# Kernel tuning notes

Hardware: AMD Instinct MI355X
Metric: run time of the kernel (lower is better)

Reference implementation:

```python
import jax, jax.numpy as jnp
import numpy as np

N_FEATURES = 1024
N_HEADS = 16
DEPTH = N_FEATURES // N_HEADS


def setup_inputs() -> dict:
    key = jax.random.key(0)
    ks = jax.random.split(key, 12)
    B, S, D = 2, 2048, N_FEATURES
    s = 1.0 / np.sqrt(D)
    return {
        "q": jax.random.normal(ks[0], (B, S, D), jnp.float32),
        "k": jax.random.normal(ks[1], (B, S, D), jnp.float32),
        "v": jax.random.normal(ks[2], (B, S, D), jnp.float32),
        "w_q": jax.random.normal(ks[3], (D, D), jnp.float32) * s,
        "b_q": jnp.zeros((D,), jnp.float32),
        "w_k": jax.random.normal(ks[4], (D, D), jnp.float32) * s,
        "b_k": jnp.zeros((D,), jnp.float32),
        "w_v": jax.random.normal(ks[5], (D, D), jnp.float32) * s,
        "b_v": jnp.zeros((D,), jnp.float32),
        "w_o": jax.random.normal(ks[6], (D, D), jnp.float32) * s,
        "b_o": jnp.zeros((D,), jnp.float32),
    }


def _split_heads(x):
    # [B, S, D] -> [B, H, S, depth]
    B, S, _ = x.shape
    return x.reshape(B, S, N_HEADS, DEPTH).transpose(0, 2, 1, 3)


def reference(q, k, v, w_q, b_q, w_k, b_k, w_v, b_v, w_o, b_o):
    B, S, D = q.shape
    qh = _split_heads(q @ w_q + b_q)  # [B,H,S,d]
    kh = _split_heads(k @ w_k + b_k)
    vh = _split_heads(v @ w_v + b_v)
    scale = 1.0 / jnp.sqrt(jnp.asarray(DEPTH, jnp.float32))
    logits = jnp.einsum("bhqd,bhkd->bhqk", qh, kh) * scale  # [B,H,S,S]
    attn_weights = jax.nn.softmax(logits, axis=-1)
    attn = jnp.einsum("bhqk,bhkd->bhqd", attn_weights, vh)
    concat = attn.transpose(0, 2, 1, 3).reshape(B, S, D)
    output = concat @ w_o + b_o
    return output, attn_weights
```

## Files before the change

### kernel.cpp

```cpp
#include <hip/hip_runtime.h>

typedef __attribute__((ext_vector_type(8))) short short8;
typedef __attribute__((ext_vector_type(4))) float f32x4;

#define MFMA_BF16(A,B,C) __builtin_amdgcn_mfma_f32_16x16x32_bf16((A),(B),(C),0,0,0)

__device__ __forceinline__ unsigned short f2bu(float f) {
  unsigned int u = __float_as_uint(f);
  u += 0x7fffu + ((u >> 16) & 1u);
  return (unsigned short)(u >> 16);
}
__device__ __forceinline__ float bu2f(unsigned short u) {
  return __uint_as_float(((unsigned int)u) << 16);
}
__device__ __forceinline__ void gload16(const void* g, void* l) {
  __builtin_amdgcn_global_load_lds(
      (const __attribute__((address_space(1))) void*)g,
      (__attribute__((address_space(3))) void*)l, 16, 0, 0);
}

__global__ __launch_bounds__(256) void cvt_bf16_kernel(const float* __restrict__ in,
                                                       unsigned short* __restrict__ out,
                                                       int n4) {
  int i = blockIdx.x * 256 + threadIdx.x;
  if (i >= n4) return;
  const float4 v = reinterpret_cast<const float4*>(in)[i];
  ushort4 o;
  o.x = f2bu(v.x); o.y = f2bu(v.y); o.z = f2bu(v.z); o.w = f2bu(v.w);
  reinterpret_cast<ushort4*>(out)[i] = o;
}

__global__ __launch_bounds__(256) void transpose_cvt_kernel(const float* __restrict__ w,
                                                            unsigned short* __restrict__ wt) {
  __shared__ float t[32][33];
  const int bx = blockIdx.x * 32;
  const int by = blockIdx.y * 32;
  const int tx = threadIdx.x & 31, ty = threadIdx.x >> 5;
  for (int j = 0; j < 4; ++j)
    t[ty + 8 * j][tx] = w[(size_t)(bx + ty + 8 * j) * 1024 + by + tx];
  __syncthreads();
  for (int j = 0; j < 4; ++j)
    wt[(size_t)(by + ty + 8 * j) * 1024 + bx + tx] = f2bu(t[tx][ty + 8 * j]);
}

template <int OUT_MODE>
__global__ __launch_bounds__(512) void gemm_bt(
    const unsigned short* __restrict__ A, const unsigned short* __restrict__ Wt,
    const float* __restrict__ bias, void* __restrict__ Cout) {
  __shared__ unsigned short g_lds[2][16384];
  const int M0 = blockIdx.x * 128, N0 = blockIdx.y * 128;
  const int tid = threadIdx.x, lane = tid & 63, wid = tid >> 6;
  const int lr = lane & 15, lg = lane >> 4;
  const int wr = wid >> 2, wc = wid & 3;
  const int srow = lane >> 3, slot = lane & 7;
  f32x4 acc[4][2];
#pragma unroll
  for (int m = 0; m < 4; ++m)
#pragma unroll
    for (int n = 0; n < 2; ++n) acc[m][n] = (f32x4){0.f, 0.f, 0.f, 0.f};

#define G_STAGE(buf, kk)                                                             \
  {                                                                                  \
    _Pragma("unroll") for (int i_ = 0; i_ < 2; ++i_) {                               \
      int idx_ = wid * 2 + i_;                                                       \
      int row_ = idx_ * 8 + srow;                                                    \
      int gs_ = slot ^ (row_ & 7);                                                   \
      gload16(&A[(size_t)(M0 + row_) * 1024 + (kk) + gs_ * 8],                       \
              (char*)&g_lds[buf][0] + idx_ * 1024);                                  \
      gload16(&Wt[(size_t)(N0 + row_) * 1024 + (kk) + gs_ * 8],                      \
              (char*)&g_lds[buf][0] + 16384 + idx_ * 1024);                          \
    }                                                                                \
  }

  G_STAGE(0, 0);
  __syncthreads();
  for (int kt = 0; kt < 16; ++kt) {
    const int cur = kt & 1;
    if (kt < 15) G_STAGE(cur ^ 1, (kt + 1) * 64);
    short8 af[4][2], bf[2][2];
#pragma unroll
    for (int m = 0; m < 4; ++m)
#pragma unroll
      for (int kh = 0; kh < 2; ++kh) {
        int row = wr * 64 + m * 16 + lr;
        int s = (kh * 4 + lg) ^ (row & 7);
        af[m][kh] = *reinterpret_cast<const short8*>((const char*)&g_lds[cur][0] + row * 128 + s * 16);
      }
#pragma unroll
    for (int n = 0; n < 2; ++n)
#pragma unroll
      for (int kh = 0; kh < 2; ++kh) {
        int row = wc * 32 + n * 16 + lr;
        int s = (kh * 4 + lg) ^ (row & 7);
        bf[n][kh] = *reinterpret_cast<const short8*>((const char*)&g_lds[cur][0] + 16384 + row * 128 + s * 16);
      }
#pragma unroll
    for (int kh = 0; kh < 2; ++kh)
#pragma unroll
      for (int m = 0; m < 4; ++m)
#pragma unroll
        for (int n = 0; n < 2; ++n)
          acc[m][n] = MFMA_BF16(af[m][kh], bf[n][kh], acc[m][n]);
    __syncthreads();
  }

  if (OUT_MODE != 2) {
#pragma unroll
    for (int m = 0; m < 4; ++m)
#pragma unroll
      for (int n = 0; n < 2; ++n)
#pragma unroll
        for (int r = 0; r < 4; ++r) {
          int grow = M0 + wr * 64 + m * 16 + lg * 4 + r;
          int gcol = N0 + wc * 32 + n * 16 + lr;
          float vv = acc[m][n][r] + bias[gcol];
          if (OUT_MODE == 1)
            reinterpret_cast<float*>(Cout)[(size_t)grow * 1024 + gcol] = vv;
          else
            reinterpret_cast<unsigned short*>(Cout)[(size_t)grow * 1024 + gcol] = f2bu(vv);
        }
  } else {
    unsigned short* t = &g_lds[0][0];
#pragma unroll
    for (int m = 0; m < 4; ++m)
#pragma unroll
      for (int n = 0; n < 2; ++n) {
        int ch = wc * 32 + n * 16 + lr;
        int s4 = wr * 64 + m * 16 + lg * 4;
        int sb = (s4 * 2) ^ ((ch & 7) << 4);
        ushort4 pk;
        pk.x = f2bu(acc[m][n][0] + bias[N0 + ch]);
        pk.y = f2bu(acc[m][n][1] + bias[N0 + ch]);
        pk.z = f2bu(acc[m][n][2] + bias[N0 + ch]);
        pk.w = f2bu(acc[m][n][3] + bias[N0 + ch]);
        *reinterpret_cast<ushort4*>((char*)t + ch * 256 + sb) = pk;
      }
    __syncthreads();
    unsigned short* Vt = (unsigned short*)Cout;
    const int ch = tid >> 2, sc = tid & 3;
    const int bb = M0 >> 11;
    unsigned short* dst = Vt + (size_t)(bb * 1024 + N0 + ch) * 2048 + (M0 & 2047) + sc * 8;
#pragma unroll
    for (int i = 0; i < 4; ++i) {
      int sb = (sc * 16 + i * 64) ^ ((ch & 7) << 4);
      short8 v = *reinterpret_cast<const short8*>((const char*)t + ch * 256 + sb);
      *reinterpret_cast<short8*>(dst + i * 32) = v;
    }
  }
#undef G_STAGE
}

__global__ __launch_bounds__(512) void attn_kernel(
    const unsigned short* __restrict__ Qp, const unsigned short* __restrict__ Kp,
    const unsigned short* __restrict__ Vt, float* __restrict__ attnw,
    unsigned short* __restrict__ attnc) {
  __shared__ unsigned short k_lds[2][4096];
  __shared__ unsigned short vt_lds[2][4096];
  __shared__ unsigned short w_lds[8][16][68];
  __shared__ float linv_lds[128];
  const int bid = blockIdx.x;
  const int qt = bid & 15, h = (bid >> 4) & 15, b = bid >> 8;
  const int tid = threadIdx.x, lane = tid & 63, wid = tid >> 6;
  const int lr = lane & 15, lg = lane >> 4;
  const int q0 = qt * 128;
  const float scale = 0.125f;
  const int srow = lane >> 3, slot = lane & 7;

  short8 aq[2];
#pragma unroll
  for (int kh = 0; kh < 2; ++kh)
    aq[kh] = *reinterpret_cast<const short8*>(
        &Qp[(size_t)(b * 2048 + q0 + wid * 16 + lr) * 1024 + h * 64 + kh * 32 + lg * 8]);

  const size_t kbase = (size_t)b * 2048 * 1024 + (size_t)(h * 64);
  const size_t vtbase = (size_t)(b * 1024 + h * 64) * 2048;

#define K_STAGE(buf, kk)                                                          \
  {                                                                               \
    int row_ = wid * 8 + srow;                                                    \
    int gs_ = slot ^ (row_ & 7);                                                  \
    gload16(&Kp[kbase + (size_t)((kk) + row_) * 1024 + gs_ * 8],                  \
            (char*)&k_lds[buf][0] + wid * 1024);                                  \
  }
#define V_STAGE(buf, kk)                                                          \
  {                                                                               \
    int row_ = wid * 8 + srow;                                                    \
    int gs_ = slot ^ (row_ & 7);                                                  \
    gload16(&Vt[vtbase + (size_t)row_ * 2048 + (kk) + gs_ * 8],                   \
            (char*)&vt_lds[buf][0] + wid * 1024);                                 \
  }

  float lsum[4] = {0.f, 0.f, 0.f, 0.f};

  K_STAGE(0, 0);
  __syncthreads();
  for (int kt = 0; kt < 32; ++kt) {
    const int cur = kt & 1;
    if (kt < 31) K_STAGE(cur ^ 1, (kt + 1) * 64);
    f32x4 lacc[4];
#pragma unroll
    for (int nt = 0; nt < 4; ++nt) lacc[nt] = (f32x4){0.f, 0.f, 0.f, 0.f};
#pragma unroll
    for (int kh = 0; kh < 2; ++kh)
#pragma unroll
      for (int nt = 0; nt < 4; ++nt) {
        int row = nt * 16 + lr;
        int s = (kh * 4 + lg) ^ (row & 7);
        short8 kb = *reinterpret_cast<const short8*>((const char*)&k_lds[cur][0] + row * 128 + s * 16);
        lacc[nt] = MFMA_BF16(aq[kh], kb, lacc[nt]);
      }
#pragma unroll
    for (int nt = 0; nt < 4; ++nt)
#pragma unroll
      for (int r = 0; r < 4; ++r)
        lsum[r] += __expf(lacc[nt][r] * scale);
    __syncthreads();
  }
  float invl[4];
#pragma unroll
  for (int r = 0; r < 4; ++r) {
    float s = lsum[r];
    s += __shfl_xor(s, 1); s += __shfl_xor(s, 2);
    s += __shfl_xor(s, 4); s += __shfl_xor(s, 8);
    float inv = 1.f / s;
    invl[r] = inv;
    if (lr == 0) linv_lds[wid * 16 + lg * 4 + r] = inv;
  }
  float inv_j[4];
#pragma unroll
  for (int j = 0; j < 4; ++j) inv_j[j] = linv_lds[wid * 16 + 4 * j + lg];

  f32x4 oacc[4];
#pragma unroll
  for (int nt = 0; nt < 4; ++nt) oacc[nt] = (f32x4){0.f, 0.f, 0.f, 0.f};

  const size_t wrowb = (size_t)((b * 16 + h) * 2048) + q0 + wid * 16;

  K_STAGE(0, 0);
  V_STAGE(0, 0);
  __syncthreads();
  for (int kt = 0; kt < 32; ++kt) {
    const int cur = kt & 1;
    const int k0 = kt * 64;
    if (kt < 31) { K_STAGE(cur ^ 1, k0 + 64); V_STAGE(cur ^ 1, k0 + 64); }
    f32x4 lacc[4];
#pragma unroll
    for (int nt = 0; nt < 4; ++nt) lacc[nt] = (f32x4){0.f, 0.f, 0.f, 0.f};
#pragma unroll
    for (int kh = 0; kh < 2; ++kh)
#pragma unroll
      for (int nt = 0; nt < 4; ++nt) {
        int row = nt * 16 + lr;
        int s = (kh * 4 + lg) ^ (row & 7);
        short8 kb = *reinterpret_cast<const short8*>((const char*)&k_lds[cur][0] + row * 128 + s * 16);
        lacc[nt] = MFMA_BF16(aq[kh], kb, lacc[nt]);
      }
#pragma unroll
    for (int nt = 0; nt < 4; ++nt)
#pragma unroll
      for (int r = 0; r < 4; ++r)
        w_lds[wid][lg * 4 + r][nt * 16 + lr] = f2bu(__expf(lacc[nt][r] * scale));
#pragma unroll
    for (int ks = 0; ks < 2; ++ks) {
      short8 wa = *reinterpret_cast<const short8*>(&w_lds[wid][lr][ks * 32 + lg * 8]);
#pragma unroll
      for (int nt = 0; nt < 4; ++nt) {
        int row = nt * 16 + lr;
        int s = (ks * 4 + lg) ^ (row & 7);
        short8 vb = *reinterpret_cast<const short8*>((const char*)&vt_lds[cur][0] + row * 128 + s * 16);
        oacc[nt] = MFMA_BF16(wa, vb, oacc[nt]);
      }
    }
#pragma unroll
    for (int j = 0; j < 4; ++j) {
      int rowl = 4 * j + lg;
      ushort4 wv = *reinterpret_cast<const ushort4*>(&w_lds[wid][rowl][lr * 4]);
      f32x4 o;
      o[0] = bu2f(wv.x) * inv_j[j];
      o[1] = bu2f(wv.y) * inv_j[j];
      o[2] = bu2f(wv.z) * inv_j[j];
      o[3] = bu2f(wv.w) * inv_j[j];
      __builtin_nontemporal_store(o, reinterpret_cast<f32x4*>(&attnw[(wrowb + rowl) * 2048 + k0 + lr * 4]));
    }
    __syncthreads();
  }
#pragma unroll
  for (int nt = 0; nt < 4; ++nt)
#pragma unroll
    for (int r = 0; r < 4; ++r) {
      int srow2 = q0 + wid * 16 + lg * 4 + r;
      attnc[(size_t)(b * 2048 + srow2) * 1024 + h * 64 + nt * 16 + lr] =
          f2bu(oacc[nt][r] * invl[r]);
    }
#undef K_STAGE
#undef V_STAGE
}

extern "C" void kernel_launch(void* const* d_in, const int* in_sizes, int n_in,
                              void* d_out, int out_size, void* d_ws, size_t ws_size,
                              hipStream_t stream) {
  const float* q = (const float*)d_in[0];
  const float* k = (const float*)d_in[1];
  const float* v = (const float*)d_in[2];
  const float* w_q = (const float*)d_in[3];
  const float* b_q = (const float*)d_in[4];
  const float* w_k = (const float*)d_in[5];
  const float* b_k = (const float*)d_in[6];
  const float* w_v = (const float*)d_in[7];
  const float* b_v = (const float*)d_in[8];
  const float* w_o = (const float*)d_in[9];
  const float* b_o = (const float*)d_in[10];

  unsigned short* ws = (unsigned short*)d_ws;
  unsigned short* Qp  = ws;
  unsigned short* Kp  = ws + 4194304;
  unsigned short* Vt  = ws + 8388608;
  unsigned short* tmp = ws + 12582912;
  unsigned short* wqt = ws + 16777216;
  unsigned short* wkt = wqt + 1048576;
  unsigned short* wvt = wkt + 1048576;
  unsigned short* wot = wvt + 1048576;

  float* outO = (float*)d_out;
  float* attnw = outO + 4194304;

  transpose_cvt_kernel<<<dim3(32, 32), 256, 0, stream>>>(w_q, wqt);
  transpose_cvt_kernel<<<dim3(32, 32), 256, 0, stream>>>(w_k, wkt);
  transpose_cvt_kernel<<<dim3(32, 32), 256, 0, stream>>>(w_v, wvt);
  transpose_cvt_kernel<<<dim3(32, 32), 256, 0, stream>>>(w_o, wot);

  cvt_bf16_kernel<<<4096, 256, 0, stream>>>(q, tmp, 1048576);
  gemm_bt<0><<<dim3(32, 8), 512, 0, stream>>>(tmp, wqt, b_q, (void*)Qp);
  cvt_bf16_kernel<<<4096, 256, 0, stream>>>(k, tmp, 1048576);
  gemm_bt<0><<<dim3(32, 8), 512, 0, stream>>>(tmp, wkt, b_k, (void*)Kp);
  cvt_bf16_kernel<<<4096, 256, 0, stream>>>(v, tmp, 1048576);
  gemm_bt<2><<<dim3(32, 8), 512, 0, stream>>>(tmp, wvt, b_v, (void*)Vt);

  attn_kernel<<<512, 512, 0, stream>>>(Qp, Kp, Vt, attnw, tmp);

  gemm_bt<1><<<dim3(32, 8), 512, 0, stream>>>(tmp, wot, b_o, d_out);
}
```

Before: 262.0 us.

## Batch conversion launches, use exp2, and cut attention loop barriers

Merges the four weight-transpose launches into one 3D-grid launch and the three input conversions into one launch. The bf16 copies of the inputs are staged in the attention-weights output buffer, which is overwritten later. The attention kernel now uses exp2f with a prescaled log2e constant and replaces two __syncthreads per iteration with a single s_waitcnt plus barrier at the top of each double-buffered iteration. This cuts launch overhead and barrier stalls, but relies on the buffers not being used concurrently and on the manual vmcnt counts matching the outstanding loads.

```diff
diff --git a/kernel.cpp b/kernel.cpp
--- a/kernel.cpp
+++ b/kernel.cpp
@@ -4,6 +4,8 @@
 typedef __attribute__((ext_vector_type(4))) float f32x4;
 
 #define MFMA_BF16(A,B,C) __builtin_amdgcn_mfma_f32_16x16x32_bf16((A),(B),(C),0,0,0)
+
+#define SCALE_LOG2E 0.18033688011112043f
 
 __device__ __forceinline__ unsigned short f2bu(float f) {
   unsigned int u = __float_as_uint(f);
@@ -18,21 +20,28 @@
       (const __attribute__((address_space(1))) void*)g,
       (__attribute__((address_space(3))) void*)l, 16, 0, 0);
 }
-
-__global__ __launch_bounds__(256) void cvt_bf16_kernel(const float* __restrict__ in,
-                                                       unsigned short* __restrict__ out,
-                                                       int n4) {
+#define WAITV0 asm volatile("s_waitcnt vmcnt(0)" ::: "memory")
+#define WAITV4 asm volatile("s_waitcnt vmcnt(4)" ::: "memory")
+__device__ __forceinline__ void barrier_fence() {
+  __builtin_amdgcn_s_barrier();
+  __builtin_amdgcn_sched_barrier(0);
+}
+
+struct Cvt3Args { const float* s[3]; unsigned short* d[3]; };
+__global__ __launch_bounds__(256) void cvt3_kernel(Cvt3Args a) {
+  const int w = blockIdx.y;
   int i = blockIdx.x * 256 + threadIdx.x;
-  if (i >= n4) return;
-  const float4 v = reinterpret_cast<const float4*>(in)[i];
+  const float4 v = reinterpret_cast<const float4*>(a.s[w])[i];
   ushort4 o;
   o.x = f2bu(v.x); o.y = f2bu(v.y); o.z = f2bu(v.z); o.w = f2bu(v.w);
-  reinterpret_cast<ushort4*>(out)[i] = o;
-}
-
-__global__ __launch_bounds__(256) void transpose_cvt_kernel(const float* __restrict__ w,
-                                                            unsigned short* __restrict__ wt) {
+  reinterpret_cast<ushort4*>(a.d[w])[i] = o;
+}
+
+struct Tr4Args { const float* s[4]; unsigned short* d[4]; };
+__global__ __launch_bounds__(256) void transpose4_kernel(Tr4Args a) {
   __shared__ float t[32][33];
+  const float* w = a.s[blockIdx.z];
+  unsigned short* wt = a.d[blockIdx.z];
   const int bx = blockIdx.x * 32;
   const int by = blockIdx.y * 32;
   const int tx = threadIdx.x & 31, ty = threadIdx.x >> 5;
@@ -163,7 +172,6 @@
   const int tid = threadIdx.x, lane = tid & 63, wid = tid >> 6;
   const int lr = lane & 15, lg = lane >> 4;
   const int q0 = qt * 128;
-  const float scale = 0.125f;
   const int srow = lane >> 3, slot = lane & 7;
 
   short8 aq[2];
@@ -193,9 +201,10 @@
   float lsum[4] = {0.f, 0.f, 0.f, 0.f};
 
   K_STAGE(0, 0);
-  __syncthreads();
   for (int kt = 0; kt < 32; ++kt) {
     const int cur = kt & 1;
+    WAITV0;
+    barrier_fence();
     if (kt < 31) K_STAGE(cur ^ 1, (kt + 1) * 64);
     f32x4 lacc[4];
 #pragma unroll
@@ -213,8 +222,7 @@
     for (int nt = 0; nt < 4; ++nt)
 #pragma unroll
       for (int r = 0; r < 4; ++r)
-        lsum[r] += __expf(lacc[nt][r] * scale);
-    __syncthreads();
+        lsum[r] += exp2f(lacc[nt][r] * SCALE_LOG2E);
   }
   float invl[4];
 #pragma unroll
@@ -236,12 +244,15 @@
 
   const size_t wrowb = (size_t)((b * 16 + h) * 2048) + q0 + wid * 16;
 
+  __syncthreads();
+
   K_STAGE(0, 0);
   V_STAGE(0, 0);
-  __syncthreads();
   for (int kt = 0; kt < 32; ++kt) {
     const int cur = kt & 1;
     const int k0 = kt * 64;
+    if (kt == 0) { WAITV0; } else { WAITV4; }
+    barrier_fence();
     if (kt < 31) { K_STAGE(cur ^ 1, k0 + 64); V_STAGE(cur ^ 1, k0 + 64); }
     f32x4 lacc[4];
 #pragma unroll
@@ -259,7 +270,7 @@
     for (int nt = 0; nt < 4; ++nt)
 #pragma unroll
       for (int r = 0; r < 4; ++r)
-        w_lds[wid][lg * 4 + r][nt * 16 + lr] = f2bu(__expf(lacc[nt][r] * scale));
+        w_lds[wid][lg * 4 + r][nt * 16 + lr] = f2bu(exp2f(lacc[nt][r] * SCALE_LOG2E));
 #pragma unroll
     for (int ks = 0; ks < 2; ++ks) {
       short8 wa = *reinterpret_cast<const short8*>(&w_lds[wid][lr][ks * 32 + lg * 8]);
@@ -282,7 +293,6 @@
       o[3] = bu2f(wv.w) * inv_j[j];
       __builtin_nontemporal_store(o, reinterpret_cast<f32x4*>(&attnw[(wrowb + rowl) * 2048 + k0 + lr * 4]));
     }
-    __syncthreads();
   }
 #pragma unroll
   for (int nt = 0; nt < 4; ++nt)
@@ -312,10 +322,10 @@
   const float* b_o = (const float*)d_in[10];
 
   unsigned short* ws = (unsigned short*)d_ws;
-  unsigned short* Qp  = ws;
-  unsigned short* Kp  = ws + 4194304;
-  unsigned short* Vt  = ws + 8388608;
-  unsigned short* tmp = ws + 12582912;
+  unsigned short* Qp    = ws;
+  unsigned short* Kp    = ws + 4194304;
+  unsigned short* Vt    = ws + 8388608;
+  unsigned short* attnc = ws + 12582912;
   unsigned short* wqt = ws + 16777216;
   unsigned short* wkt = wqt + 1048576;
   unsigned short* wvt = wkt + 1048576;
@@ -324,19 +334,25 @@
   float* outO = (float*)d_out;
   float* attnw = outO + 4194304;
 
-  transpose_cvt_kernel<<<dim3(32, 32), 256, 0, stream>>>(w_q, wqt);
-  transpose_cvt_kernel<<<dim3(32, 32), 256, 0, stream>>>(w_k, wkt);
-  transpose_cvt_kernel<<<dim3(32, 32), 256, 0, stream>>>(w_v, wvt);
-  transpose_cvt_kernel<<<dim3(32, 32), 256, 0, stream>>>(w_o, wot);
-
-  cvt_bf16_kernel<<<4096, 256, 0, stream>>>(q, tmp, 1048576);
-  gemm_bt<0><<<dim3(32, 8), 512, 0, stream>>>(tmp, wqt, b_q, (void*)Qp);
-  cvt_bf16_kernel<<<4096, 256, 0, stream>>>(k, tmp, 1048576);
-  gemm_bt<0><<<dim3(32, 8), 512, 0, stream>>>(tmp, wkt, b_k, (void*)Kp);
-  cvt_bf16_kernel<<<4096, 256, 0, stream>>>(v, tmp, 1048576);
-  gemm_bt<2><<<dim3(32, 8), 512, 0, stream>>>(tmp, wvt, b_v, (void*)Vt);
-
-  attn_kernel<<<512, 512, 0, stream>>>(Qp, Kp, Vt, attnw, tmp);
-
-  gemm_bt<1><<<dim3(32, 8), 512, 0, stream>>>(tmp, wot, b_o, d_out);
-}
+  unsigned short* qb = (unsigned short*)attnw;
+  unsigned short* kb = qb + 4194304;
+  unsigned short* vb = kb + 4194304;
+
+  Tr4Args ta;
+  ta.s[0] = w_q; ta.s[1] = w_k; ta.s[2] = w_v; ta.s[3] = w_o;
+  ta.d[0] = wqt; ta.d[1] = wkt; ta.d[2] = wvt; ta.d[3] = wot;
+  transpose4_kernel<<<dim3(32, 32, 4), 256, 0, stream>>>(ta);
+
+  Cvt3Args ca;
+  ca.s[0] = q; ca.s[1] = k; ca.s[2] = v;
+  ca.d[0] = qb; ca.d[1] = kb; ca.d[2] = vb;
+  cvt3_kernel<<<dim3(4096, 3), 256, 0, stream>>>(ca);
+
+  gemm_bt<0><<<dim3(32, 8), 512, 0, stream>>>(qb, wqt, b_q, (void*)Qp);
+  gemm_bt<0><<<dim3(32, 8), 512, 0, stream>>>(kb, wkt, b_k, (void*)Kp);
+  gemm_bt<2><<<dim3(32, 8), 512, 0, stream>>>(vb, wvt, b_v, (void*)Vt);
+
+  attn_kernel<<<512, 512, 0, stream>>>(Qp, Kp, Vt, attnw, attnc);
+
+  gemm_bt<1><<<dim3(32, 8), 512, 0, stream>>>(attnc, wot, b_o, d_out);
+}
```

Result: faster. 244.2 us (-6.8%).
